# Kernel tuning notes

Measured on AMD Instinct MI355X. Metric: run time of the kernel, lower is better.

The kernel has to match this reference:

```python
import jax, jax.numpy as jnp
import numpy as np

EPS = 1e-8


def setup_inputs() -> dict:
    key = jax.random.key(0)
    k1, k2, k3, k4, k5 = jax.random.split(key, 5)
    B, D, N, M = 16, 128, 2048, 2048
    return {
        "src_embedding": jax.random.normal(k1, (B, D, N), dtype=jnp.float32),
        "tgt_embedding": jax.random.normal(k2, (B, D, M), dtype=jnp.float32),
        "src": jax.random.normal(k3, (B, 3, N), dtype=jnp.float32),
        "tgt": jax.random.normal(k4, (B, 3, M), dtype=jnp.float32),
        "temperature": jax.random.uniform(k5, (B, 1), dtype=jnp.float32),
    }


def reference(src_embedding, tgt_embedding, src, tgt, temperature):
    B = src.shape[0]
    # cross-attention scores [B, N, M] and row softmax
    scores = jax.nn.softmax(
        jnp.einsum("bdn,bdm->bnm", src_embedding, tgt_embedding), axis=-1
    )
    # hard correspondence: argmax over tgt points, gather tgt coords -> [B, 3, N]
    idx = jnp.argmax(scores, axis=-1)                      # [B, N]
    src_corr = jnp.take_along_axis(tgt, idx[:, None, :].repeat(3, axis=1), axis=-1)
    # entropy-based weights (note: original applies -1/(entropy+eps), kept faithfully)
    w = jnp.sum(scores * jnp.log(scores + EPS), axis=-1)   # [B, N]
    w = -1.0 / (w + EPS)
    w_norm = w / (jnp.sum(w, axis=-1, keepdims=True) + EPS)  # [B, N]
    wn = w_norm[:, None, :]                                # [B, 1, N]
    src_centroid = jnp.sum(src * wn, axis=2, keepdims=True)       # [B, 3, 1]
    tgt_centroid = jnp.sum(src_corr * wn, axis=2, keepdims=True)  # [B, 3, 1]
    src_centered = src - src_centroid
    corr_centered = (src_corr - tgt_centroid) * wn
    # 3x3 cross-covariance per batch
    H = jnp.einsum("bin,bjn->bij", src_centered, corr_centered) + jnp.eye(3, dtype=src.dtype) * EPS
    # batched 3x3 SVD entirely on device; torch.svd returns V s.t. H = U S V^T
    U, S, Vh = jnp.linalg.svd(H)
    V = jnp.swapaxes(Vh, -1, -2)
    r = jnp.einsum("bij,bkj->bik", V, U)                   # V @ U^T
    det = jnp.linalg.det(r)                                # [B]
    diag = jnp.tile(jnp.eye(3, dtype=src.dtype), (B, 1, 1)).at[:, 2, 2].set(det)
    R = jnp.einsum("bij,bjk,blk->bil", V, diag, U)         # V @ diag @ U^T
    t = (jnp.einsum("bij,bjk->bik", -R, src_centroid) + tgt_centroid).reshape(B, 3)
    return R, t, scores
```

## Files before the change

kernel.cpp:

```cpp
#include <hip/hip_runtime.h>
#include <math.h>

constexpr int B = 16, D = 128, N = 2048, M = 2048;
#define EPSF 1e-8f

__global__ __launch_bounds__(256) void gemm_logits(
    const float* __restrict__ Ae, const float* __restrict__ Be,
    float* __restrict__ out)
{
    const int b  = blockIdx.z;
    const int n0 = blockIdx.y * 128;
    const int m0 = blockIdx.x * 128;
    const float* A  = Ae + (size_t)b * D * N;
    const float* Bm = Be + (size_t)b * D * M;
    float* C = out + (size_t)b * N * M;

    __shared__ float As[8][128];
    __shared__ float Bs[8][128];

    const int t  = threadIdx.x;
    const int lr = t >> 5;
    const int lc = (t & 31) * 4;
    const int tx = t & 15;
    const int ty = t >> 4;

    const float* Aptr = A  + (size_t)lr * N + n0 + lc;
    const float* Bptr = Bm + (size_t)lr * M + m0 + lc;

    float acc[8][8];
#pragma unroll
    for (int i = 0; i < 8; ++i)
#pragma unroll
        for (int j = 0; j < 8; ++j) acc[i][j] = 0.f;

    float4 av = *(const float4*)(Aptr);
    float4 bv = *(const float4*)(Bptr);

    for (int d0 = 0; d0 < D; d0 += 8) {
        *(float4*)(&As[lr][lc]) = av;
        *(float4*)(&Bs[lr][lc]) = bv;
        __syncthreads();
        if (d0 + 8 < D) {
            av = *(const float4*)(Aptr + (size_t)(d0 + 8) * N);
            bv = *(const float4*)(Bptr + (size_t)(d0 + 8) * M);
        }
#pragma unroll
        for (int kk = 0; kk < 8; ++kk) {
            float a[8], bb[8];
            *(float4*)(&a[0])  = *(const float4*)(&As[kk][ty * 4]);
            *(float4*)(&a[4])  = *(const float4*)(&As[kk][64 + ty * 4]);
            *(float4*)(&bb[0]) = *(const float4*)(&Bs[kk][tx * 4]);
            *(float4*)(&bb[4]) = *(const float4*)(&Bs[kk][64 + tx * 4]);
#pragma unroll
            for (int i = 0; i < 8; ++i)
#pragma unroll
                for (int j = 0; j < 8; ++j)
                    acc[i][j] = fmaf(a[i], bb[j], acc[i][j]);
        }
        __syncthreads();
    }

#pragma unroll
    for (int i = 0; i < 8; ++i) {
        const int row = (i < 4) ? (ty * 4 + i) : (64 + ty * 4 + (i - 4));
        float4 c0 = make_float4(acc[i][0], acc[i][1], acc[i][2], acc[i][3]);
        float4 c1 = make_float4(acc[i][4], acc[i][5], acc[i][6], acc[i][7]);
        size_t base = (size_t)(n0 + row) * M + m0;
        *(float4*)(C + base + tx * 4)      = c0;
        *(float4*)(C + base + 64 + tx * 4) = c1;
    }
}

__global__ __launch_bounds__(256) void softmax_rows(
    float* __restrict__ scores, float* __restrict__ wout, int* __restrict__ idxout)
{
    const int row = blockIdx.x;
    float* p = scores + (size_t)row * M;
    const int t = threadIdx.x;
    const int wid = t >> 6;

    float4 v0 = ((const float4*)p)[t];
    float4 v1 = ((const float4*)p)[t + 256];
    float vals[8] = {v0.x, v0.y, v0.z, v0.w, v1.x, v1.y, v1.z, v1.w};
    int   idxs[8] = {t*4, t*4+1, t*4+2, t*4+3,
                     1024 + t*4, 1024 + t*4 + 1, 1024 + t*4 + 2, 1024 + t*4 + 3};

    float m = vals[0]; int mi = idxs[0];
#pragma unroll
    for (int k = 1; k < 8; ++k)
        if (vals[k] > m) { m = vals[k]; mi = idxs[k]; }

    __shared__ float sv[256];
    __shared__ int   si[256];
    __shared__ float resf[2];
    __shared__ int   resi;

    sv[t] = m; si[t] = mi;
    __syncthreads();
    if (t < 128) {
        float ov = sv[t + 128]; int oi = si[t + 128];
        if (ov > m || (ov == m && oi < mi)) { m = ov; mi = oi; }
    }
    if (wid == 1) { sv[t] = m; si[t] = mi; }
    __syncthreads();
    if (t < 64) {
        float ov = sv[t + 64]; int oi = si[t + 64];
        if (ov > m || (ov == m && oi < mi)) { m = ov; mi = oi; }
#pragma unroll
        for (int s = 32; s > 0; s >>= 1) {
            float om = __shfl_down(m, s);
            int   oi2 = __shfl_down(mi, s);
            if (om > m || (om == m && oi2 < mi)) { m = om; mi = oi2; }
        }
        if (t == 0) { resf[0] = m; resi = mi; }
    }
    __syncthreads();
    const float rowmax = resf[0];
    const int   rowidx = resi;

    float e[8]; float lsum = 0.f;
#pragma unroll
    for (int k = 0; k < 8; ++k) { e[k] = expf(vals[k] - rowmax); lsum += e[k]; }
    sv[t] = lsum;
    __syncthreads();
    float sum = lsum;
    if (t < 128) sum = sum + sv[t + 128];
    if (wid == 1) sv[t] = sum;
    __syncthreads();
    if (t < 64) {
        sum = sum + sv[t + 64];
#pragma unroll
        for (int s = 32; s > 0; s >>= 1) sum = sum + __shfl_down(sum, s);
        if (t == 0) resf[1] = sum;
    }
    __syncthreads();
    const float inv = 1.0f / resf[1];

    float ent = 0.f;
#pragma unroll
    for (int k = 0; k < 8; ++k) {
        float pk = e[k] * inv;
        e[k] = pk;
        ent += pk * logf(pk + EPSF);
    }
    ((float4*)p)[t]       = make_float4(e[0], e[1], e[2], e[3]);
    ((float4*)p)[t + 256] = make_float4(e[4], e[5], e[6], e[7]);

    sv[t] = ent;
    __syncthreads();
    if (t < 128) ent = ent + sv[t + 128];
    if (wid == 1) sv[t] = ent;
    __syncthreads();
    if (t < 64) {
        ent = ent + sv[t + 64];
#pragma unroll
        for (int s = 32; s > 0; s >>= 1) ent = ent + __shfl_down(ent, s);
        if (t == 0) {
            wout[row]   = -1.0f / (ent + EPSF);
            idxout[row] = rowidx;
        }
    }
}

template <int Q>
__device__ inline void block_sum_hybrid(float (&v)[Q], float (*red)[256],
                                        float* res, int t, int wid)
{
#pragma unroll
    for (int q = 0; q < Q; ++q) red[q][t] = v[q];
    __syncthreads();
    if (t < 128) {
#pragma unroll
        for (int q = 0; q < Q; ++q) v[q] += red[q][t + 128];
    }
    if (wid == 1) {
#pragma unroll
        for (int q = 0; q < Q; ++q) red[q][t] = v[q];
    }
    __syncthreads();
    if (t < 64) {
#pragma unroll
        for (int q = 0; q < Q; ++q) v[q] += red[q][t + 64];
#pragma unroll
        for (int s = 32; s > 0; s >>= 1)
#pragma unroll
            for (int q = 0; q < Q; ++q) v[q] += __shfl_down(v[q], s);
        if (t == 0) {
#pragma unroll
            for (int q = 0; q < Q; ++q) res[q] = v[q];
        }
    }
    __syncthreads();
#pragma unroll
    for (int q = 0; q < Q; ++q) v[q] = res[q];
}

__global__ __launch_bounds__(256) void kabsch(
    const float* __restrict__ src, const float* __restrict__ tgt,
    const float* __restrict__ wraw, const int* __restrict__ idxv,
    float* __restrict__ Rout, float* __restrict__ tout)
{
    const int b = blockIdx.x;
    const int t = threadIdx.x;
    const int wid = t >> 6;
    const float* S  = src  + (size_t)b * 3 * N;
    const float* T  = tgt  + (size_t)b * 3 * M;
    const float* w  = wraw + (size_t)b * N;
    const int*  idx = idxv + (size_t)b * N;

    __shared__ float red[9][256];
    __shared__ float res[9];

    float w8[8]; int i8[8];
    float s8[8][3], g8[8][3];
    float lsum[1] = {0.f};
#pragma unroll
    for (int k = 0; k < 8; ++k) {
        int n = t + 256 * k;
        w8[k] = w[n];
        i8[k] = idx[n];
        lsum[0] += w8[k];
#pragma unroll
        for (int i = 0; i < 3; ++i) {
            s8[k][i] = S[i * N + n];
            g8[k][i] = T[i * M + i8[k]];
        }
    }
    block_sum_hybrid<1>(lsum, red, res, t, wid);
    const float W = lsum[0] + EPSF;

    float c[6] = {0, 0, 0, 0, 0, 0};
#pragma unroll
    for (int k = 0; k < 8; ++k) {
        float wn = w8[k] / W;
#pragma unroll
        for (int i = 0; i < 3; ++i) {
            c[i]     += wn * s8[k][i];
            c[3 + i] += wn * g8[k][i];
        }
    }
    block_sum_hybrid<6>(c, red, res, t, wid);
    float cen[6];
#pragma unroll
    for (int i = 0; i < 6; ++i) cen[i] = c[i];

    float h[9] = {0};
#pragma unroll
    for (int k = 0; k < 8; ++k) {
        float wn = w8[k] / W;
        float a0 = s8[k][0] - cen[0], a1 = s8[k][1] - cen[1], a2 = s8[k][2] - cen[2];
        float b0 = (g8[k][0] - cen[3]) * wn;
        float b1 = (g8[k][1] - cen[4]) * wn;
        float b2 = (g8[k][2] - cen[5]) * wn;
        h[0] += a0 * b0; h[1] += a0 * b1; h[2] += a0 * b2;
        h[3] += a1 * b0; h[4] += a1 * b1; h[5] += a1 * b2;
        h[6] += a2 * b0; h[7] += a2 * b1; h[8] += a2 * b2;
    }
    block_sum_hybrid<9>(h, red, res, t, wid);

    if (t == 0) {
        float hr[9];
#pragma unroll
        for (int q = 0; q < 9; ++q) hr[q] = h[q];

        double H[3][3];
        for (int i = 0; i < 3; ++i)
            for (int j = 0; j < 3; ++j)
                H[i][j] = (double)hr[i * 3 + j] + (i == j ? 1e-8 : 0.0);

        double A[3][3];
        for (int i = 0; i < 3; ++i)
            for (int j = 0; j < 3; ++j)
                A[i][j] = H[0][i] * H[0][j] + H[1][i] * H[1][j] + H[2][i] * H[2][j];

        double V[3][3] = {{1, 0, 0}, {0, 1, 0}, {0, 0, 1}};
        const int PP[3] = {0, 0, 1}, QQ[3] = {1, 2, 2};
        for (int sweep = 0; sweep < 30; ++sweep) {
            for (int r = 0; r < 3; ++r) {
                int p = PP[r], q = QQ[r];
                double apq = A[p][q];
                if (fabs(apq) < 1e-300) continue;
                double theta = (A[q][q] - A[p][p]) / (2.0 * apq);
                double tt = (theta >= 0 ? 1.0 : -1.0) /
                            (fabs(theta) + sqrt(theta * theta + 1.0));
                double cc = 1.0 / sqrt(tt * tt + 1.0);
                double ss = tt * cc;
                for (int k = 0; k < 3; ++k) {
                    double akp = A[k][p], akq = A[k][q];
                    A[k][p] = cc * akp - ss * akq;
                    A[k][q] = ss * akp + cc * akq;
                }
                for (int k = 0; k < 3; ++k) {
                    double apk = A[p][k], aqk = A[q][k];
                    A[p][k] = cc * apk - ss * aqk;
                    A[q][k] = ss * apk + cc * aqk;
                }
                for (int k = 0; k < 3; ++k) {
                    double vkp = V[k][p], vkq = V[k][q];
                    V[k][p] = cc * vkp - ss * vkq;
                    V[k][q] = ss * vkp + cc * vkq;
                }
            }
        }
        double ev[3] = {A[0][0], A[1][1], A[2][2]};
        int ord[3] = {0, 1, 2};
        for (int i = 0; i < 2; ++i)
            for (int j = i + 1; j < 3; ++j)
                if (ev[ord[j]] > ev[ord[i]]) { int tmp = ord[i]; ord[i] = ord[j]; ord[j] = tmp; }
        double Vs[3][3];
        for (int i = 0; i < 3; ++i)
            for (int j = 0; j < 3; ++j)
                Vs[i][j] = V[i][ord[j]];

        double U[3][3];
        for (int j = 0; j < 2; ++j) {
            double u0 = H[0][0] * Vs[0][j] + H[0][1] * Vs[1][j] + H[0][2] * Vs[2][j];
            double u1 = H[1][0] * Vs[0][j] + H[1][1] * Vs[1][j] + H[1][2] * Vs[2][j];
            double u2 = H[2][0] * Vs[0][j] + H[2][1] * Vs[1][j] + H[2][2] * Vs[2][j];
            if (j == 1) {
                double d0 = u0 * U[0][0] + u1 * U[1][0] + u2 * U[2][0];
                u0 -= d0 * U[0][0]; u1 -= d0 * U[1][0]; u2 -= d0 * U[2][0];
            }
            double nn = sqrt(u0 * u0 + u1 * u1 + u2 * u2);
            if (nn < 1e-150) {
                u0 = (j == 0) ? 1.0 : -U[1][0];
                u1 = (j == 0) ? 0.0 : U[0][0];
                u2 = 0.0;
                nn = sqrt(u0 * u0 + u1 * u1 + u2 * u2);
                if (nn < 1e-150) { u0 = 0; u1 = 0; u2 = 1; nn = 1; }
            }
            U[0][j] = u0 / nn; U[1][j] = u1 / nn; U[2][j] = u2 / nn;
        }
        U[0][2] = U[1][0] * U[2][1] - U[2][0] * U[1][1];
        U[1][2] = U[2][0] * U[0][1] - U[0][0] * U[2][1];
        U[2][2] = U[0][0] * U[1][1] - U[1][0] * U[0][1];

        double r[3][3];
        for (int i = 0; i < 3; ++i)
            for (int j = 0; j < 3; ++j)
                r[i][j] = Vs[i][0] * U[j][0] + Vs[i][1] * U[j][1] + Vs[i][2] * U[j][2];
        double det = r[0][0] * (r[1][1] * r[2][2] - r[1][2] * r[2][1])
                   - r[0][1] * (r[1][0] * r[2][2] - r[1][2] * r[2][0])
                   + r[0][2] * (r[1][0] * r[2][1] - r[1][1] * r[2][0]);

        double R[3][3];
        for (int i = 0; i < 3; ++i)
            for (int j = 0; j < 3; ++j)
                R[i][j] = Vs[i][0] * U[j][0] + Vs[i][1] * U[j][1] + det * Vs[i][2] * U[j][2];

        double tv[3];
        for (int i = 0; i < 3; ++i)
            tv[i] = (double)cen[3 + i]
                  - (R[i][0] * cen[0] + R[i][1] * cen[1] + R[i][2] * cen[2]);

        for (int i = 0; i < 3; ++i)
            for (int j = 0; j < 3; ++j)
                Rout[b * 9 + i * 3 + j] = (float)R[i][j];
        for (int i = 0; i < 3; ++i)
            tout[b * 3 + i] = (float)tv[i];
    }
}

extern "C" void kernel_launch(void* const* d_in, const int* in_sizes, int n_in,
                              void* d_out, int out_size, void* d_ws, size_t ws_size,
                              hipStream_t stream)
{
    const float* src_emb = (const float*)d_in[0];
    const float* tgt_emb = (const float*)d_in[1];
    const float* src     = (const float*)d_in[2];
    const float* tgt     = (const float*)d_in[3];

    float* out    = (float*)d_out;
    float* Rout   = out;
    float* tout   = out + B * 9;
    float* scores = out + B * 12;

    float* wws   = (float*)d_ws;
    int*   idxws = (int*)((float*)d_ws + B * N);

    dim3 g1(M / 128, N / 128, B);
    gemm_logits<<<g1, 256, 0, stream>>>(src_emb, tgt_emb, scores);
    softmax_rows<<<B * N, 256, 0, stream>>>(scores, wws, idxws);
    kabsch<<<B, 256, 0, stream>>>(src, tgt, wws, idxws, Rout, tout);
}
```

Before: 562.5 us.

## Double-buffer GEMM shared tiles with K-step 16 and one barrier per iteration

The logits GEMM now stages 16 rows of the reduction dimension per iteration instead of 8. It ping-pongs between two shared-memory buffers, which lets it drop the trailing __syncthreads so each K-step has a single barrier. This halves the number of barriers and loop iterations and keeps more register-prefetched data in flight. The cost is four times the shared memory per block and more live prefetch registers, which may reduce occupancy.

```diff
diff --git a/kernel.cpp b/kernel.cpp
--- a/kernel.cpp
+++ b/kernel.cpp
@@ -15,8 +15,8 @@
     const float* Bm = Be + (size_t)b * D * M;
     float* C = out + (size_t)b * N * M;
 
-    __shared__ float As[8][128];
-    __shared__ float Bs[8][128];
+    __shared__ float As[2][16][128];
+    __shared__ float Bs[2][16][128];
 
     const int t  = threadIdx.x;
     const int lr = t >> 5;
@@ -33,31 +33,38 @@
 #pragma unroll
         for (int j = 0; j < 8; ++j) acc[i][j] = 0.f;
 
-    float4 av = *(const float4*)(Aptr);
-    float4 bv = *(const float4*)(Bptr);
-
-    for (int d0 = 0; d0 < D; d0 += 8) {
-        *(float4*)(&As[lr][lc]) = av;
-        *(float4*)(&Bs[lr][lc]) = bv;
+    float4 av0 = *(const float4*)(Aptr);
+    float4 av1 = *(const float4*)(Aptr + (size_t)8 * N);
+    float4 bv0 = *(const float4*)(Bptr);
+    float4 bv1 = *(const float4*)(Bptr + (size_t)8 * M);
+
+    int buf = 0;
+    for (int d0 = 0; d0 < D; d0 += 16) {
+        *(float4*)(&As[buf][lr][lc])     = av0;
+        *(float4*)(&As[buf][lr + 8][lc]) = av1;
+        *(float4*)(&Bs[buf][lr][lc])     = bv0;
+        *(float4*)(&Bs[buf][lr + 8][lc]) = bv1;
         __syncthreads();
-        if (d0 + 8 < D) {
-            av = *(const float4*)(Aptr + (size_t)(d0 + 8) * N);
-            bv = *(const float4*)(Bptr + (size_t)(d0 + 8) * M);
-        }
-#pragma unroll
-        for (int kk = 0; kk < 8; ++kk) {
+        if (d0 + 16 < D) {
+            av0 = *(const float4*)(Aptr + (size_t)(d0 + 16) * N);
+            av1 = *(const float4*)(Aptr + (size_t)(d0 + 24) * N);
+            bv0 = *(const float4*)(Bptr + (size_t)(d0 + 16) * M);
+            bv1 = *(const float4*)(Bptr + (size_t)(d0 + 24) * M);
+        }
+#pragma unroll
+        for (int kk = 0; kk < 16; ++kk) {
             float a[8], bb[8];
-            *(float4*)(&a[0])  = *(const float4*)(&As[kk][ty * 4]);
-            *(float4*)(&a[4])  = *(const float4*)(&As[kk][64 + ty * 4]);
-            *(float4*)(&bb[0]) = *(const float4*)(&Bs[kk][tx * 4]);
-            *(float4*)(&bb[4]) = *(const float4*)(&Bs[kk][64 + tx * 4]);
+            *(float4*)(&a[0])  = *(const float4*)(&As[buf][kk][ty * 4]);
+            *(float4*)(&a[4])  = *(const float4*)(&As[buf][kk][64 + ty * 4]);
+            *(float4*)(&bb[0]) = *(const float4*)(&Bs[buf][kk][tx * 4]);
+            *(float4*)(&bb[4]) = *(const float4*)(&Bs[buf][kk][64 + tx * 4]);
 #pragma unroll
             for (int i = 0; i < 8; ++i)
 #pragma unroll
                 for (int j = 0; j < 8; ++j)
                     acc[i][j] = fmaf(a[i], bb[j], acc[i][j]);
         }
-        __syncthreads();
+        buf ^= 1;
     }
 
 #pragma unroll
```

Measured after the change: 568.7 us. No clear change (+1.1%).
